# Kernel tuning notes

Hardware: AMD Instinct MI355X
Metric: run time of the kernel (lower is better)

## Reference

```python
import jax, jax.numpy as jnp
import numpy as np

N, E = 50000, 800000
D_IN, HID, H, C, E_DIM = 128, 128, 4, 32, 32  # C = HID // H


def setup_inputs() -> dict:
    key = jax.random.key(0)
    ks = jax.random.split(key, 16)
    def lin(k, fan_in, fan_out):
        return jax.random.normal(k, (fan_in, fan_out), jnp.float32) / np.sqrt(fan_in)
    return {
        "x": jax.random.normal(ks[0], (N, D_IN), jnp.float32),
        "edge_index": jax.random.randint(ks[1], (2, E), 0, N, jnp.int32),
        "edge_attr": jax.random.normal(ks[2], (E, E_DIM), jnp.float32),
        # TransformerConv params (bias=True on q/k/v and skip; lin_edge has no bias in PyG)
        "Wq": lin(ks[3], D_IN, HID), "bq": jnp.zeros((HID,), jnp.float32),
        "Wk": lin(ks[4], D_IN, HID), "bk": jnp.zeros((HID,), jnp.float32),
        "Wv": lin(ks[5], D_IN, HID), "bv": jnp.zeros((HID,), jnp.float32),
        "We": lin(ks[6], E_DIM, HID),
        "Wskip": lin(ks[7], D_IN, HID), "bskip": jnp.zeros((HID,), jnp.float32),
        # MLP([HID, HID, HID]) -> two Linear layers, GELU(tanh) after each (plain_last=False)
        "W1": lin(ks[8], HID, HID), "b1": jnp.zeros((HID,), jnp.float32),
        "W2": lin(ks[9], HID, HID), "b2": jnp.zeros((HID,), jnp.float32),
    }


def reference(x, edge_index, edge_attr, Wq, bq, Wk, bk, Wv, bv, We, Wskip, bskip, W1, b1, W2, b2):
    src, dst = edge_index[0], edge_index[1]  # messages flow src(j) -> dst(i)
    n = x.shape[0]
    q = (x @ Wq + bq).reshape(n, H, C)
    k = (x @ Wk + bk).reshape(n, H, C)
    v = (x @ Wv + bv).reshape(n, H, C)
    e = (edge_attr @ We).reshape(-1, H, C)          # [E,H,C]
    kj = k[src] + e                                  # gather + edge lift
    vj = v[src] + e
    alpha = jnp.einsum("ehc,ehc->eh", q[dst], kj) / np.sqrt(C)  # [E,H]
    # segment softmax over destination neighborhoods (PyG softmax semantics)
    amax = jax.ops.segment_max(alpha, dst, num_segments=n)      # [N,H]
    amax = jnp.where(jnp.isfinite(amax), amax, 0.0)
    ex = jnp.exp(alpha - amax[dst])
    denom = jax.ops.segment_sum(ex, dst, num_segments=n)
    alpha = ex / (denom[dst] + 1e-16)
    # (attention dropout p=0.3 is inactive in eval mode)
    agg = jax.ops.segment_sum(vj * alpha[:, :, None], dst, num_segments=n)  # [N,H,C]
    out = agg.reshape(n, HID) + (x @ Wskip + bskip)  # concat heads + root skip
    # residual MLP: gelu(tanh) after every layer since plain_last=False, norm=None
    h = jax.nn.gelu(out @ W1 + b1, approximate=True)
    h = jax.nn.gelu(h @ W2 + b2, approximate=True)
    return out + h
```

## Files before the change

### kernel.cpp

```cpp
#include <hip/hip_runtime.h>
#include <math.h>


#define D 128
#define EDIM 32

using bf16x8 = __attribute__((ext_vector_type(8))) short;
using f32x4  = __attribute__((ext_vector_type(4))) float;
using ushort8 = __attribute__((ext_vector_type(8))) unsigned short;

__device__ inline unsigned short f2bf(float f) {
    unsigned int u = __float_as_uint(f);
    u += 0x7FFFu + ((u >> 16) & 1u);
    return (unsigned short)(u >> 16);
}
__device__ inline float bf2f(unsigned short h) {
    return __uint_as_float(((unsigned int)h) << 16);
}
__device__ inline float gelu_fast(float x) {
    float x3 = x * x * x;
    float u = 0.7978845608028654f * (x + 0.044715f * x3);
    float t = 1.f - 2.f / (__expf(2.f * u) + 1.f);
    return 0.5f * x * (1.f + t);
}
__device__ inline float quad_add(float x) {
    int a = __builtin_amdgcn_update_dpp(0, __float_as_int(x), 0xB1, 0xF, 0xF, true);
    x += __int_as_float(a);
    a = __builtin_amdgcn_update_dpp(0, __float_as_int(x), 0x4E, 0xF, 0xF, true);
    x += __int_as_float(a);
    return x;
}

__device__ inline bf16x8 ldsB(const unsigned short* sw, int col, int kk0) {
    return *(const bf16x8*)(sw + col * 128 + (kk0 ^ ((col & 7) << 3)));
}

__global__ __launch_bounds__(256) void prep_kernel(
    const float* __restrict__ Wq, const float* __restrict__ Wk,
    const float* __restrict__ Wv, const float* __restrict__ Wsk,
    const float* __restrict__ W1, const float* __restrict__ W2,
    const float* __restrict__ We, const float* __restrict__ bq,
    unsigned short* __restrict__ Wt, float* __restrict__ bqE,
    const int* __restrict__ EI, int* __restrict__ deg, int E, int HB,
    const float* __restrict__ x, unsigned short* __restrict__ XB, long xtot)
{
    if ((int)blockIdx.x >= 513 + HB) {
        long i8 = ((long)(blockIdx.x - 513 - HB) * 256 + threadIdx.x) * 8;
        if (i8 + 8 <= xtot) {
            float4 a = *(const float4*)(x + i8);
            float4 b = *(const float4*)(x + i8 + 4);
            ushort8 u;
            u[0] = f2bf(a.x); u[1] = f2bf(a.y); u[2] = f2bf(a.z); u[3] = f2bf(a.w);
            u[4] = f2bf(b.x); u[5] = f2bf(b.y); u[6] = f2bf(b.z); u[7] = f2bf(b.w);
            *(ushort8*)(XB + i8) = u;
        }
        return;
    }
    if (blockIdx.x >= 513) {
        int e = (blockIdx.x - 513) * 256 + threadIdx.x;
        if (e < E) atomicAdd(&deg[EI[E + e]], 1);
        return;
    }
    int t = blockIdx.x * 256 + threadIdx.x;
    int m = t >> 14;
    int r = t & 16383;
    if (m >= 8) {
        if (r < 128) {
            const int hb = r & 96, k = r & 31;
            const float* wek = We + (size_t)k * D + hb;
            float s = 0.f;
#pragma unroll 8
            for (int c = 0; c < 32; ++c) s = fmaf(bq[hb + c], wek[c], s);
            bqE[r] = s;
        }
        return;
    }
    int col = r & 127, kk = r >> 7;
    float v;
    if (m < 6) {
        const float* W = (m == 0) ? Wq : (m == 1) ? Wk : (m == 2) ? Wv
                       : (m == 3) ? Wsk : (m == 4) ? W1 : W2;
        v = W[(size_t)kk * D + col];
    } else if (m == 6) {
        const int hb = col & 96;
        const float* wqr = Wq + (size_t)kk * D + hb;
        const float* wer = We + (size_t)(col & 31) * D + hb;
        float s = 0.f;
#pragma unroll 8
        for (int c = 0; c < 32; ++c) s = fmaf(wqr[c], wer[c], s);
        v = s;
    } else {
        v = ((kk >> 5) == (col >> 5)) ? We[(size_t)(kk & 31) * D + col] : 0.f;
    }
    Wt[(size_t)m * 16384 + (size_t)col * 128 + (kk ^ ((col & 7) << 3))] = f2bf(v);
}

__global__ __launch_bounds__(1024) void scanA(
    const int* __restrict__ deg, int* __restrict__ rowptr,
    int* __restrict__ psums, int N)
{
    __shared__ int tmp[1024];
    const int t = threadIdx.x;
    const int i = blockIdx.x * 1024 + t;
    int v = (i < N) ? deg[i] : 0;
    tmp[t] = v;
    __syncthreads();
    for (int off = 1; off < 1024; off <<= 1) {
        int add = (t >= off) ? tmp[t - off] : 0;
        __syncthreads();
        tmp[t] += add;
        __syncthreads();
    }
    if (i < N) rowptr[i + 1] = tmp[t];
    if (t == 1023) psums[blockIdx.x] = tmp[1023];
}

__global__ __launch_bounds__(1024) void scanB(int* __restrict__ psums, int nb)
{
    __shared__ int tmp[1024];
    const int t = threadIdx.x;
    int v = (t < nb) ? psums[t] : 0;
    tmp[t] = v;
    __syncthreads();
    for (int off = 1; off < 1024; off <<= 1) {
        int add = (t >= off) ? tmp[t - off] : 0;
        __syncthreads();
        tmp[t] += add;
        __syncthreads();
    }
    if (t < nb) psums[t] = tmp[t] - v;
}

__global__ __launch_bounds__(256) void scanC(
    int* __restrict__ rowptr, int* __restrict__ cursor,
    const int* __restrict__ psums, int N)
{
    int i = blockIdx.x * 256 + threadIdx.x;
    if (i == 0) { rowptr[0] = 0; cursor[0] = 0; }
    if (i < N) {
        int val = rowptr[i + 1] + psums[i >> 10];
        rowptr[i + 1] = val;
        if (i + 1 < N) cursor[i + 1] = val;
    }
}

__global__ __launch_bounds__(256) void scatter_kernel(
    const int* __restrict__ EI, int* __restrict__ cursor,
    int2* __restrict__ SE, int E)
{
    int e = blockIdx.x * 256 + threadIdx.x;
    if (e < E) {
        int dst = EI[E + e];
        int pos = atomicAdd(&cursor[dst], 1);
        SE[pos] = make_int2(EI[e], e);
    }
}

__global__ __launch_bounds__(256) void gemm5(
    const unsigned short* __restrict__ XB, const unsigned short* __restrict__ Wt,
    const float* __restrict__ bq, const float* __restrict__ bk,
    const float* __restrict__ bv, const float* __restrict__ bs,
    const float* __restrict__ bqE,
    unsigned short* __restrict__ QA, unsigned short* __restrict__ KV,
    float* __restrict__ S, int N, int NB2)
{
    __shared__ unsigned short sw[16384];
    const int t = threadIdx.x;
    const int bid = blockIdx.x;
    const int m = bid / NB2;
    const int bx = bid - m * NB2;
    const int widx = (m < 4) ? m : 6;
    const int lane = t & 63;
    const int w = t >> 6;
    const int row0 = bx * 128 + w * 32;
    const int lrow = lane & 15;
    const int kb = (lane >> 4) * 8;
    const int rq = (lane >> 4) * 4;

    const unsigned short* gsrc = Wt + (size_t)widx * 16384;
    ushort8 stg[8];
#pragma unroll
    for (int it = 0; it < 8; ++it)
        stg[it] = *(const ushort8*)(gsrc + (t + it * 256) * 8);

    bf16x8 af0[4], af1[4];
    {
        int a0 = row0 + lrow;      if (a0 > N - 1) a0 = N - 1;
        int a1 = row0 + 16 + lrow; if (a1 > N - 1) a1 = N - 1;
        const unsigned short* x0 = XB + (size_t)a0 * D + kb;
        const unsigned short* x1 = XB + (size_t)a1 * D + kb;
#pragma unroll
        for (int kf = 0; kf < 4; ++kf) {
            af0[kf] = *(const bf16x8*)(x0 + kf * 32);
            af1[kf] = *(const bf16x8*)(x1 + kf * 32);
        }
    }

#pragma unroll
    for (int it = 0; it < 8; ++it)
        *(ushort8*)(&sw[(t + it * 256) * 8]) = stg[it];
    __syncthreads();

    const float* bias = (m == 0) ? bq : (m == 1) ? bk : (m == 2) ? bv
                      : (m == 3) ? bs : bqE;
    f32x4 acc0[8], acc1[8];
#pragma unroll
    for (int nf = 0; nf < 8; ++nf) {
        acc0[nf] = (f32x4){0.f, 0.f, 0.f, 0.f};
        acc1[nf] = (f32x4){0.f, 0.f, 0.f, 0.f};
    }
#pragma unroll
    for (int nf = 0; nf < 8; ++nf) {
        const int col = nf * 16 + lrow;
#pragma unroll
        for (int kf = 0; kf < 4; ++kf) {
            bf16x8 bfr = ldsB(sw, col, kf * 32 + kb);
            acc0[nf] = __builtin_amdgcn_mfma_f32_16x16x32_bf16(af0[kf], bfr, acc0[nf], 0, 0, 0);
            acc1[nf] = __builtin_amdgcn_mfma_f32_16x16x32_bf16(af1[kf], bfr, acc1[nf], 0, 0, 0);
        }
    }

    if (m == 3) {
#pragma unroll
        for (int rb = 0; rb < 2; ++rb) {
#pragma unroll
            for (int nf = 0; nf < 8; ++nf) {
                const int col = nf * 16 + lrow;
                const float bb = bias[col];
#pragma unroll
                for (int i = 0; i < 4; ++i) {
                    int r = row0 + rb * 16 + rq + i;
                    if (r < N)
                        S[(size_t)r * D + col] = ((rb == 0) ? acc0[nf][i] : acc1[nf][i]) + bb;
                }
            }
        }
        return;
    }

    __syncthreads();
#pragma unroll
    for (int rb = 0; rb < 2; ++rb) {
#pragma unroll
        for (int nf = 0; nf < 8; ++nf) {
            const int col = nf * 16 + lrow;
            const float bb = bias[col];
#pragma unroll
            for (int i = 0; i < 4; ++i)
                sw[(w * 32 + rb * 16 + rq + i) * 128 + col] =
                    f2bf(((rb == 0) ? acc0[nf][i] : acc1[nf][i]) + bb);
        }
    }
    unsigned short* gout = (m == 0) ? QA : (m == 1) ? KV
                         : (m == 2) ? KV + 128 : QA + 128;
#pragma unroll
    for (int it = 0; it < 8; ++it) {
        const int gidx = it * 64 + lane;
        const int row_l = gidx >> 4;
        const int chk = gidx & 15;
        const int r = row0 + row_l;
        ushort8 vv = *(const ushort8*)(&sw[(w * 32 + row_l) * 128 + chk * 8]);
        if (r < N) *(ushort8*)(gout + (size_t)r * 256 + chk * 8) = vv;
    }
}

__global__ __launch_bounds__(256) void gather_pass(
    const int* __restrict__ rowptr, const int2* __restrict__ SE,
    const float* __restrict__ EA,
    const unsigned short* __restrict__ QA, const unsigned short* __restrict__ KV,
    float* __restrict__ SB, unsigned short* __restrict__ SAS, int N)
{
    const int lane = threadIdx.x & 63;
    const int wid = threadIdx.x >> 6;
    const int n = blockIdx.x * 4 + wid;
    if (n >= N) return;
    const int g = lane & 15;
    const int grp = lane >> 4;
    const int eoff = (g & 3) * 8;

    float q8[8], qe8[8];
    {
        const unsigned short* qa = QA + (size_t)n * 256 + g * 8;
        bf16x8 qb  = *(const bf16x8*)(qa);
        bf16x8 qeb = *(const bf16x8*)(qa + 128);
#pragma unroll
        for (int j = 0; j < 8; ++j) {
            q8[j]  = bf2f((unsigned short)qb[j]);
            qe8[j] = bf2f((unsigned short)qeb[j]);
        }
    }

    float acc[8], sa[8], den = 0.f;
#pragma unroll
    for (int j = 0; j < 8; ++j) { acc[j] = 0.f; sa[j] = 0.f; }

    const int i0 = rowptr[n], i1 = rowptr[n + 1];

    int2 se[4];
#pragma unroll
    for (int u = 0; u < 4; ++u) {
        int ii = i0 + grp + u * 4;
        se[u] = (ii < i1) ? SE[ii] : make_int2(-1, 0);
    }

    for (int base = i0; base < i1; base += 16) {
        bf16x8 kS[4], vS[4];
        float4 e0S[4], e1S[4];
#pragma unroll
        for (int u = 0; u < 4; ++u) {
            kS[u] = (bf16x8){0,0,0,0,0,0,0,0};
            vS[u] = kS[u];
            e0S[u] = (float4){0.f,0.f,0.f,0.f};
            e1S[u] = e0S[u];
            if (se[u].x >= 0) {
                const unsigned short* kv = KV + (size_t)se[u].x * 256 + g * 8;
                kS[u] = *(const bf16x8*)(kv);
                vS[u] = *(const bf16x8*)(kv + 128);
                const float* ear = EA + (size_t)se[u].y * EDIM + eoff;
                e0S[u] = *(const float4*)(ear);
                e1S[u] = *(const float4*)(ear + 4);
            }
        }
        int2 seN[4];
#pragma unroll
        for (int u = 0; u < 4; ++u) {
            int ii = base + 16 + grp + u * 4;
            seN[u] = (ii < i1) ? SE[ii] : make_int2(-1, 0);
        }
#pragma unroll
        for (int u = 0; u < 4; ++u) {
            float ef[8] = {e0S[u].x, e0S[u].y, e0S[u].z, e0S[u].w,
                           e1S[u].x, e1S[u].y, e1S[u].z, e1S[u].w};
            float p = 0.f;
#pragma unroll
            for (int j = 0; j < 8; ++j)
                p = fmaf(q8[j], bf2f((unsigned short)kS[u][j]),
                         fmaf(ef[j], qe8[j], p));
            p = quad_add(p);
            const float ex = (se[u].x >= 0) ? __expf(p * 0.17677669529663689f) : 0.f;
            den += ex;
#pragma unroll
            for (int j = 0; j < 8; ++j) {
                acc[j] = fmaf(ex, bf2f((unsigned short)vS[u][j]), acc[j]);
                sa[j]  = fmaf(ex, ef[j], sa[j]);
            }
        }
#pragma unroll
        for (int u = 0; u < 4; ++u) se[u] = seN[u];
    }

#pragma unroll
    for (int off = 16; off <= 32; off <<= 1) {
        den += __shfl_xor(den, off, 64);
#pragma unroll
        for (int j = 0; j < 8; ++j) {
            acc[j] += __shfl_xor(acc[j], off, 64);
            sa[j]  += __shfl_xor(sa[j],  off, 64);
        }
    }

    if (grp == 0) {
        const float rden = 1.f / (den + 1e-16f);
        float* so = SB + (size_t)n * D + g * 8;
        unsigned short* po = SAS + (size_t)n * D + g * 8;
#pragma unroll
        for (int j = 0; j < 8; ++j) {
            so[j] = fmaf(acc[j], rden, so[j]);
            po[j] = f2bf(sa[j] * rden);
        }
    }
}

__global__ __launch_bounds__(256) void fused_mlp(
    const float* __restrict__ SB, const unsigned short* __restrict__ SAS,
    const unsigned short* __restrict__ WtC, const unsigned short* __restrict__ Wt1,
    const unsigned short* __restrict__ Wt2,
    const float* __restrict__ b1, const float* __restrict__ b2,
    float* __restrict__ FINAL, int N)
{
    __shared__ unsigned short sw[16384];
    __shared__ unsigned short bounce[64 * 136];
    const int t = threadIdx.x;
    const int lane = t & 63;
    const int w = t >> 6;
    const int row0 = blockIdx.x * 64 + w * 16;
    const int lrow = lane & 15;
    const int kb = (lane >> 4) * 8;
    const int rq = (lane >> 4) * 4;

    ushort8 stg[8];
#pragma unroll
    for (int it = 0; it < 8; ++it)
        stg[it] = *(const ushort8*)(WtC + (t + it * 256) * 8);

    bf16x8 af[4];
    {
        int ar = row0 + lrow; if (ar > N - 1) ar = N - 1;
        const unsigned short* xr = SAS + (size_t)ar * D + kb;
#pragma unroll
        for (int kf = 0; kf < 4; ++kf) af[kf] = *(const bf16x8*)(xr + kf * 32);
    }
    f32x4 out[8];
#pragma unroll
    for (int nf = 0; nf < 8; ++nf) {
        const int col = nf * 16 + lrow;
#pragma unroll
        for (int i = 0; i < 4; ++i) {
            int r = row0 + rq + i;
            out[nf][i] = (r < N) ? SB[(size_t)r * D + col] : 0.f;
        }
    }
#pragma unroll
    for (int it = 0; it < 8; ++it)
        *(ushort8*)(&sw[(t + it * 256) * 8]) = stg[it];
    __syncthreads();

#pragma unroll
    for (int nf = 0; nf < 8; ++nf) {
        const int col = nf * 16 + lrow;
#pragma unroll
        for (int kf = 0; kf < 4; ++kf)
            out[nf] = __builtin_amdgcn_mfma_f32_16x16x32_bf16(
                af[kf], ldsB(sw, col, kf * 32 + kb), out[nf], 0, 0, 0);
    }
    __syncthreads();

#pragma unroll
    for (int it = 0; it < 8; ++it)
        stg[it] = *(const ushort8*)(Wt1 + (t + it * 256) * 8);
#pragma unroll
    for (int nf = 0; nf < 8; ++nf) {
        const int col = nf * 16 + lrow;
#pragma unroll
        for (int i = 0; i < 4; ++i)
            bounce[(w * 16 + rq + i) * 136 + col] = f2bf(out[nf][i]);
    }
#pragma unroll
    for (int it = 0; it < 8; ++it)
        *(ushort8*)(&sw[(t + it * 256) * 8]) = stg[it];
    __syncthreads();

    bf16x8 af2[4];
#pragma unroll
    for (int kf = 0; kf < 4; ++kf)
        af2[kf] = *(const bf16x8*)(&bounce[(w * 16 + lrow) * 136 + kb + kf * 32]);
    f32x4 acc2[8];
#pragma unroll
    for (int nf = 0; nf < 8; ++nf) acc2[nf] = (f32x4){0.f, 0.f, 0.f, 0.f};
#pragma unroll
    for (int nf = 0; nf < 8; ++nf) {
        const int col = nf * 16 + lrow;
#pragma unroll
        for (int kf = 0; kf < 4; ++kf)
            acc2[nf] = __builtin_amdgcn_mfma_f32_16x16x32_bf16(
                af2[kf], ldsB(sw, col, kf * 32 + kb), acc2[nf], 0, 0, 0);
    }
    __syncthreads();

#pragma unroll
    for (int it = 0; it < 8; ++it)
        stg[it] = *(const ushort8*)(Wt2 + (t + it * 256) * 8);
#pragma unroll
    for (int nf = 0; nf < 8; ++nf) {
        const int col = nf * 16 + lrow;
        const float bb = b1[col];
#pragma unroll
        for (int i = 0; i < 4; ++i)
            bounce[(w * 16 + rq + i) * 136 + col] = f2bf(gelu_fast(acc2[nf][i] + bb));
    }
#pragma unroll
    for (int it = 0; it < 8; ++it)
        *(ushort8*)(&sw[(t + it * 256) * 8]) = stg[it];
    __syncthreads();

    bf16x8 af3[4];
#pragma unroll
    for (int kf = 0; kf < 4; ++kf)
        af3[kf] = *(const bf16x8*)(&bounce[(w * 16 + lrow) * 136 + kb + kf * 32]);
    f32x4 acc3[8];
#pragma unroll
    for (int nf = 0; nf < 8; ++nf) acc3[nf] = (f32x4){0.f, 0.f, 0.f, 0.f};
#pragma unroll
    for (int nf = 0; nf < 8; ++nf) {
        const int col = nf * 16 + lrow;
#pragma unroll
        for (int kf = 0; kf < 4; ++kf)
            acc3[nf] = __builtin_amdgcn_mfma_f32_16x16x32_bf16(
                af3[kf], ldsB(sw, col, kf * 32 + kb), acc3[nf], 0, 0, 0);
    }
#pragma unroll
    for (int nf = 0; nf < 8; ++nf) {
        const int col = nf * 16 + lrow;
        const float bb = b2[col];
#pragma unroll
        for (int i = 0; i < 4; ++i) {
            int r = row0 + rq + i;
            if (r < N)
                FINAL[(size_t)r * D + col] = out[nf][i] + gelu_fast(acc3[nf][i] + bb);
        }
    }
}

extern "C" void kernel_launch(void* const* d_in, const int* in_sizes, int n_in,
                              void* d_out, int out_size, void* d_ws, size_t ws_size,
                              hipStream_t stream)
{
    const float* x   = (const float*)d_in[0];
    const int*   EI  = (const int*)  d_in[1];
    const float* EA  = (const float*)d_in[2];
    const float* Wq  = (const float*)d_in[3];
    const float* bq  = (const float*)d_in[4];
    const float* Wk  = (const float*)d_in[5];
    const float* bk  = (const float*)d_in[6];
    const float* Wv  = (const float*)d_in[7];
    const float* bv  = (const float*)d_in[8];
    const float* We  = (const float*)d_in[9];
    const float* Wsk = (const float*)d_in[10];
    const float* bsk = (const float*)d_in[11];
    const float* W1  = (const float*)d_in[12];
    const float* b1  = (const float*)d_in[13];
    const float* W2  = (const float*)d_in[14];
    const float* b2  = (const float*)d_in[15];

    const int N = in_sizes[0] / D;
    const int E = in_sizes[1] / 2;

    char* p = (char*)d_ws;
    auto alloc = [&](size_t bytes) -> void* {
        void* r = (void*)p;
        p += (bytes + 255) & ~(size_t)255;
        return r;
    };
    float*          Sb     = (float*)         alloc((size_t)N * D * 4);
    unsigned short* QAb    = (unsigned short*)alloc((size_t)N * 256 * 2);
    unsigned short* KVb    = (unsigned short*)alloc((size_t)N * 256 * 2);
    unsigned short* SASb   = (unsigned short*)alloc((size_t)N * D * 2);
    unsigned short* XBb    = (unsigned short*)alloc((size_t)N * D * 2);
    int2*           SEb    = (int2*)          alloc((size_t)E * 8);
    unsigned short* Wt     = (unsigned short*)alloc((size_t)8 * 16384 * 2);
    float*          bqEb   = (float*)         alloc((size_t)128 * 4);
    int*            deg    = (int*)           alloc((size_t)N * 4);
    int*            rowptr = (int*)           alloc((size_t)(N + 1) * 4);
    int*            cursor = (int*)           alloc((size_t)(N + 1) * 4);
    int*            psums  = (int*)           alloc((size_t)1024 * 4);

    hipMemsetAsync(deg, 0, (size_t)N * sizeof(int), stream);

    const long xtot = (long)N * D;
    const int NB  = (N + 63) / 64;
    const int NB2 = (N + 127) / 128;
    const int EB  = (E + 255) / 256;
    const int XB_ = (int)((xtot + 2047) / 2048);
    const int SB_ = (N + 1023) / 1024;

    prep_kernel<<<513 + EB + XB_, 256, 0, stream>>>(
        Wq, Wk, Wv, Wsk, W1, W2, We, bq, Wt, bqEb, EI, deg, E, EB, x, XBb, xtot);

    scanA<<<SB_, 1024, 0, stream>>>(deg, rowptr, psums, N);
    scanB<<<1, 1024, 0, stream>>>(psums, SB_);
    scanC<<<(N + 255) / 256, 256, 0, stream>>>(rowptr, cursor, psums, N);

    scatter_kernel<<<EB, 256, 0, stream>>>(EI, cursor, SEb, E);

    gemm5<<<5 * NB2, 256, 0, stream>>>(
        XBb, Wt, bq, bk, bv, bsk, bqEb, QAb, KVb, Sb, N, NB2);

    gather_pass<<<(N + 3) / 4, 256, 0, stream>>>(
        rowptr, SEb, EA, QAb, KVb, Sb, SASb, N);

    fused_mlp<<<NB, 256, 0, stream>>>(Sb, SASb,
                                      Wt + (size_t)7 * 16384,
                                      Wt + (size_t)4 * 16384,
                                      Wt + (size_t)5 * 16384,
                                      b1, b2, (float*)d_out, N);
}
```

Measured before the change: 254.5 us.

## Permute edge attributes into CSR order as bf16 during scatter

The scatter kernel now writes a dst-sorted copy of edge_attr converted to bf16, plus a plain int source array, in place of the (src, edge id) pairs. The gather pass then reads edge features contiguously in CSR order at half the width instead of randomly gathering fp32 rows by original edge id. The cost is an extra full read and write of edge_attr in the scatter kernel, plus bf16 rounding of the edge features.

```diff
diff --git a/kernel.cpp b/kernel.cpp
--- a/kernel.cpp
+++ b/kernel.cpp
@@ -145,14 +145,24 @@
 }
 
 __global__ __launch_bounds__(256) void scatter_kernel(
-    const int* __restrict__ EI, int* __restrict__ cursor,
-    int2* __restrict__ SE, int E)
+    const int* __restrict__ EI, const float* __restrict__ EA,
+    int* __restrict__ cursor, int* __restrict__ srcs,
+    unsigned short* __restrict__ EAP, int E)
 {
     int e = blockIdx.x * 256 + threadIdx.x;
-    if (e < E) {
-        int dst = EI[E + e];
-        int pos = atomicAdd(&cursor[dst], 1);
-        SE[pos] = make_int2(EI[e], e);
+    if (e >= E) return;
+    int dst = EI[E + e];
+    int pos = atomicAdd(&cursor[dst], 1);
+    srcs[pos] = EI[e];
+    const float4* s4 = (const float4*)(EA + (size_t)e * EDIM);
+    unsigned short* op = EAP + (size_t)pos * EDIM;
+#pragma unroll
+    for (int j = 0; j < 4; ++j) {
+        float4 a = s4[2 * j], b = s4[2 * j + 1];
+        ushort8 u;
+        u[0] = f2bf(a.x); u[1] = f2bf(a.y); u[2] = f2bf(a.z); u[3] = f2bf(a.w);
+        u[4] = f2bf(b.x); u[5] = f2bf(b.y); u[6] = f2bf(b.z); u[7] = f2bf(b.w);
+        *(ushort8*)(op + j * 8) = u;
     }
 }
 
@@ -265,8 +275,8 @@
 }
 
 __global__ __launch_bounds__(256) void gather_pass(
-    const int* __restrict__ rowptr, const int2* __restrict__ SE,
-    const float* __restrict__ EA,
+    const int* __restrict__ rowptr, const int* __restrict__ srcs,
+    const unsigned short* __restrict__ EAP,
     const unsigned short* __restrict__ QA, const unsigned short* __restrict__ KV,
     float* __restrict__ SB, unsigned short* __restrict__ SAS, int N)
 {
@@ -296,48 +306,45 @@
 
     const int i0 = rowptr[n], i1 = rowptr[n + 1];
 
-    int2 se[4];
+    int src[4];
 #pragma unroll
     for (int u = 0; u < 4; ++u) {
         int ii = i0 + grp + u * 4;
-        se[u] = (ii < i1) ? SE[ii] : make_int2(-1, 0);
+        src[u] = (ii < i1) ? srcs[ii] : -1;
     }
 
     for (int base = i0; base < i1; base += 16) {
-        bf16x8 kS[4], vS[4];
-        float4 e0S[4], e1S[4];
+        bf16x8 kS[4], vS[4], eS[4];
 #pragma unroll
         for (int u = 0; u < 4; ++u) {
             kS[u] = (bf16x8){0,0,0,0,0,0,0,0};
             vS[u] = kS[u];
-            e0S[u] = (float4){0.f,0.f,0.f,0.f};
-            e1S[u] = e0S[u];
-            if (se[u].x >= 0) {
-                const unsigned short* kv = KV + (size_t)se[u].x * 256 + g * 8;
+            eS[u] = kS[u];
+            if (src[u] >= 0) {
+                const unsigned short* kv = KV + (size_t)src[u] * 256 + g * 8;
                 kS[u] = *(const bf16x8*)(kv);
                 vS[u] = *(const bf16x8*)(kv + 128);
-                const float* ear = EA + (size_t)se[u].y * EDIM + eoff;
-                e0S[u] = *(const float4*)(ear);
-                e1S[u] = *(const float4*)(ear + 4);
+                eS[u] = *(const bf16x8*)(EAP + (size_t)(base + grp + u * 4) * EDIM + eoff);
             }
         }
-        int2 seN[4];
+        int srcN[4];
 #pragma unroll
         for (int u = 0; u < 4; ++u) {
             int ii = base + 16 + grp + u * 4;
-            seN[u] = (ii < i1) ? SE[ii] : make_int2(-1, 0);
+            srcN[u] = (ii < i1) ? srcs[ii] : -1;
         }
 #pragma unroll
         for (int u = 0; u < 4; ++u) {
-            float ef[8] = {e0S[u].x, e0S[u].y, e0S[u].z, e0S[u].w,
-                           e1S[u].x, e1S[u].y, e1S[u].z, e1S[u].w};
+            float ef[8];
             float p = 0.f;
 #pragma unroll
-            for (int j = 0; j < 8; ++j)
+            for (int j = 0; j < 8; ++j) {
+                ef[j] = bf2f((unsigned short)eS[u][j]);
                 p = fmaf(q8[j], bf2f((unsigned short)kS[u][j]),
                          fmaf(ef[j], qe8[j], p));
+            }
             p = quad_add(p);
-            const float ex = (se[u].x >= 0) ? __expf(p * 0.17677669529663689f) : 0.f;
+            const float ex = (src[u] >= 0) ? __expf(p * 0.17677669529663689f) : 0.f;
             den += ex;
 #pragma unroll
             for (int j = 0; j < 8; ++j) {
@@ -346,7 +353,7 @@
             }
         }
 #pragma unroll
-        for (int u = 0; u < 4; ++u) se[u] = seN[u];
+        for (int u = 0; u < 4; ++u) src[u] = srcN[u];
     }
 
 #pragma unroll
@@ -536,7 +543,8 @@
     unsigned short* KVb    = (unsigned short*)alloc((size_t)N * 256 * 2);
     unsigned short* SASb   = (unsigned short*)alloc((size_t)N * D * 2);
     unsigned short* XBb    = (unsigned short*)alloc((size_t)N * D * 2);
-    int2*           SEb    = (int2*)          alloc((size_t)E * 8);
+    unsigned short* EAPb   = (unsigned short*)alloc((size_t)E * EDIM * 2);
+    int*            srcsb  = (int*)           alloc((size_t)E * 4);
     unsigned short* Wt     = (unsigned short*)alloc((size_t)8 * 16384 * 2);
     float*          bqEb   = (float*)         alloc((size_t)128 * 4);
     int*            deg    = (int*)           alloc((size_t)N * 4);
@@ -560,13 +568,13 @@
     scanB<<<1, 1024, 0, stream>>>(psums, SB_);
     scanC<<<(N + 255) / 256, 256, 0, stream>>>(rowptr, cursor, psums, N);
 
-    scatter_kernel<<<EB, 256, 0, stream>>>(EI, cursor, SEb, E);
+    scatter_kernel<<<EB, 256, 0, stream>>>(EI, EA, cursor, srcsb, EAPb, E);
 
     gemm5<<<5 * NB2, 256, 0, stream>>>(
         XBb, Wt, bq, bk, bv, bsk, bqEb, QAb, KVb, Sb, N, NB2);
 
     gather_pass<<<(N + 3) / 4, 256, 0, stream>>>(
-        rowptr, SEb, EA, QAb, KVb, Sb, SASb, N);
+        rowptr, srcsb, EAPb, QAb, KVb, Sb, SASb, N);
 
     fused_mlp<<<NB, 256, 0, stream>>>(Sb, SASb,
                                       Wt + (size_t)7 * 16384,
```

Result: no change. 259.4 us (+1.9%).
